# Kernel tuning notes

Hardware: AMD Instinct MI355X
Metric: run time of the kernel (lower is better)

## Reference

```python
import jax, jax.numpy as jnp
import numpy as np

N = 50000   # nodes
E = 800000  # edges
F = 64      # edge_feat_dim == input node dim
H0, H1 = 128, 64  # hidden_dims
OUT = 2
EPS = 1e-5


def _glorot(key, shape):
    limit = float(np.sqrt(6.0 / (shape[0] + shape[1])))
    return jax.random.uniform(key, shape, minval=-limit, maxval=limit, dtype=jnp.float32)


def _layer_norm(h, g, b):
    m = jnp.mean(h, axis=-1, keepdims=True)
    v = jnp.var(h, axis=-1, keepdims=True)
    return (h - m) * jax.lax.rsqrt(v + EPS) * g + b


def setup_inputs() -> dict:
    key = jax.random.key(0)
    ks = jax.random.split(key, 10)
    x = jax.random.normal(ks[0], (N, F), dtype=jnp.float32)
    edge_index = jax.random.randint(ks[1], (2, E), 0, N, dtype=jnp.int64)
    edge_attr = jax.random.normal(ks[2], (E, F), dtype=jnp.float32)
    # conv layer 0: Linear(F + F -> H0); conv layer 1: Linear(H0 + F -> H1)
    W0 = _glorot(ks[3], (F + F, H0)); b0 = jnp.zeros((H0,), jnp.float32)
    W1 = _glorot(ks[4], (H0 + F, H1)); b1 = jnp.zeros((H1,), jnp.float32)
    g0 = jnp.ones((H0,), jnp.float32); be0 = jnp.zeros((H0,), jnp.float32)
    g1 = jnp.ones((H1,), jnp.float32); be1 = jnp.zeros((H1,), jnp.float32)
    # classifier: Linear(2*H1 -> H1) -> ReLU -> Linear(H1 -> OUT)
    Wc0 = _glorot(ks[5], (2 * H1, H1)); bc0 = jnp.zeros((H1,), jnp.float32)
    Wc1 = _glorot(ks[6], (H1, OUT)); bc1 = jnp.zeros((OUT,), jnp.float32)
    return dict(x=x, edge_index=edge_index, edge_attr=edge_attr,
                W0=W0, b0=b0, g0=g0, be0=be0,
                W1=W1, b1=b1, g1=g1, be1=be1,
                Wc0=Wc0, bc0=bc0, Wc1=Wc1, bc1=bc1)


def reference(x, edge_index, edge_attr, W0, b0, g0, be0, W1, b1, g1, be1, Wc0, bc0, Wc1, bc1):
    src, dst = edge_index[0], edge_index[1]
    # scatter-mean of edge_attr per destination node (same for both layers,
    # since edge_attr never changes -> compute once)
    agg_sum = jax.ops.segment_sum(edge_attr, dst, num_segments=N)  # [N, F]
    cnt = jax.ops.segment_sum(jnp.ones((E, 1), x.dtype), dst, num_segments=N)
    agg = agg_sum / jnp.maximum(cnt, 1.0)
    # layer 0: cat -> linear -> relu -> layernorm (dropout is identity at eval)
    h = jax.nn.relu(jnp.concatenate([x, agg], axis=-1) @ W0 + b0)
    h = _layer_norm(h, g0, be0)
    # layer 1
    h = jax.nn.relu(jnp.concatenate([h, agg], axis=-1) @ W1 + b1)
    z = _layer_norm(h, g1, be1)  # [N, H1]
    # edge classifier: gather src/dst embeddings, concat, MLP
    edge_emb = jnp.concatenate([z[src], z[dst]], axis=-1)  # [E, 2*H1]
    hidden = jax.nn.relu(edge_emb @ Wc0 + bc0)
    return hidden @ Wc1 + bc1  # [E, OUT]
```

## Files before the change

kernel.cpp:

```cpp
#include <hip/hip_runtime.h>
#include <hip/hip_bf16.h>

#define N_NODES 50000
#define N_EDGES 800000
#define EPS 1e-5f
#define SCAN_BLOCKS 49

typedef __attribute__((ext_vector_type(8))) short short8;
typedef __attribute__((ext_vector_type(4))) float f32x4;

static __device__ __forceinline__ unsigned short f2bf(float f) {
  union { float f; unsigned u; } v; v.f = f;
  const unsigned r = v.u + 0x7FFF + ((v.u >> 16) & 1);
  return (unsigned short)(r >> 16);
}

__global__ void __launch_bounds__(256) k_prepw(
    const float* __restrict__ W0, const float* __restrict__ W1,
    const float* __restrict__ Wc0,
    unsigned short* __restrict__ W0T, unsigned short* __restrict__ W1T,
    unsigned short* __restrict__ Wc0T) {
  const int idx = blockIdx.x * 256 + threadIdx.x;
  if (idx < 128 * 128) {
    const int n = idx >> 7, k = idx & 127;
    W0T[idx] = f2bf(W0[k * 128 + n]);
  }
  if (idx < 64 * 192) {
    const int n = idx / 192, k = idx - n * 192;
    W1T[idx] = f2bf(W1[k * 64 + n]);
  }
  if (idx < 64 * 128) {
    const int n = idx >> 7, k = idx & 127;
    Wc0T[idx] = f2bf(Wc0[k * 64 + n]);
  }
}

__global__ void __launch_bounds__(256) k_zero(int* __restrict__ cnt) {
  const int base = blockIdx.x * 1024 + threadIdx.x * 4;
  if (base + 3 < N_NODES) {
    *(int4*)(cnt + base) = make_int4(0, 0, 0, 0);
  } else {
    for (int i = 0; i < 4; ++i)
      if (base + i < N_NODES) cnt[base + i] = 0;
  }
}

__global__ void k_count(const int* __restrict__ ei, int* __restrict__ cnt) {
  const int e = blockIdx.x * blockDim.x + threadIdx.x;
  if (e < N_EDGES) atomicAdd(&cnt[ei[N_EDGES + e]], 1);
}

__global__ void __launch_bounds__(256) k_scan_blk(const int* __restrict__ cnt,
                                                  int* __restrict__ starts,
                                                  int* __restrict__ bsum) {
  __shared__ int lds[256];
  const int t = threadIdx.x, b = blockIdx.x;
  const int base = b * 1024 + t * 4;
  int c0 = 0, c1 = 0, c2 = 0, c3 = 0;
  if (base + 3 < N_NODES) {
    const int4 c = *(const int4*)(cnt + base);
    c0 = c.x; c1 = c.y; c2 = c.z; c3 = c.w;
  } else {
    if (base + 0 < N_NODES) c0 = cnt[base + 0];
    if (base + 1 < N_NODES) c1 = cnt[base + 1];
    if (base + 2 < N_NODES) c2 = cnt[base + 2];
    if (base + 3 < N_NODES) c3 = cnt[base + 3];
  }
  const int s = c0 + c1 + c2 + c3;
  lds[t] = s;
  __syncthreads();
  for (int off = 1; off < 256; off <<= 1) {
    const int v = (t >= off) ? lds[t - off] : 0;
    __syncthreads();
    lds[t] += v;
    __syncthreads();
  }
  int run = lds[t] - s;
  if (t == 255) bsum[b] = lds[255];
  const int o0 = run; run += c0;
  const int o1 = run; run += c1;
  const int o2 = run; run += c2;
  const int o3 = run;
  if (base + 3 < N_NODES) {
    *(int4*)(starts + base) = make_int4(o0, o1, o2, o3);
  } else {
    if (base + 0 < N_NODES) starts[base + 0] = o0;
    if (base + 1 < N_NODES) starts[base + 1] = o1;
    if (base + 2 < N_NODES) starts[base + 2] = o2;
    if (base + 3 < N_NODES) starts[base + 3] = o3;
  }
}

__global__ void __launch_bounds__(64) k_scan_top(int* __restrict__ bsum) {
  const int t = threadIdx.x;
  int v = (t < SCAN_BLOCKS) ? bsum[t] : 0;
  const int orig = v;
  for (int off = 1; off < 64; off <<= 1) {
    const int u = __shfl_up(v, off);
    if (t >= off) v += u;
  }
  if (t < SCAN_BLOCKS) bsum[t] = v - orig;
}

__global__ void __launch_bounds__(256) k_scan_add(int* __restrict__ starts,
                                                  int* __restrict__ pos,
                                                  const int* __restrict__ bsum) {
  const int t = threadIdx.x, b = blockIdx.x;
  const int off = bsum[b];
  const int base = b * 1024 + t * 4;
  if (base + 3 < N_NODES) {
    int4 v = *(const int4*)(starts + base);
    v.x += off; v.y += off; v.z += off; v.w += off;
    *(int4*)(starts + base) = v;
    *(int4*)(pos + base) = v;
  } else {
    for (int i = 0; i < 4; ++i)
      if (base + i < N_NODES) {
        const int v = starts[base + i] + off;
        starts[base + i] = v;
        pos[base + i] = v;
      }
  }
  if (b == 0 && t == 0) starts[N_NODES] = N_EDGES;
}

__global__ void k_place(const int* __restrict__ ei, int* __restrict__ pos,
                        int* __restrict__ csr) {
  const int e = blockIdx.x * blockDim.x + threadIdx.x;
  if (e < N_EDGES) {
    const int d = ei[N_EDGES + e];
    const int slot = atomicAdd(&pos[d], 1);
    csr[slot] = e;
  }
}

__global__ void __launch_bounds__(256) k_gather(const float* __restrict__ ea,
                                                const int* __restrict__ csr,
                                                const int* __restrict__ starts,
                                                unsigned short* __restrict__ aggb) {
  const int lane = threadIdx.x & 63;
  const int wv = threadIdx.x >> 6;
  const int wstride = gridDim.x * 4;
  for (int n = blockIdx.x * 4 + wv; n < N_NODES; n += wstride) {
    const int s0 = starts[n], s1 = starts[n + 1];
    float sum = 0.0f;
    int i = s0;
    for (; i + 3 < s1; i += 4) {
      const int e0 = csr[i], e1 = csr[i + 1], e2 = csr[i + 2], e3 = csr[i + 3];
      const float a0 = ea[(size_t)e0 * 64 + lane];
      const float a1 = ea[(size_t)e1 * 64 + lane];
      const float a2 = ea[(size_t)e2 * 64 + lane];
      const float a3 = ea[(size_t)e3 * 64 + lane];
      sum += (a0 + a1) + (a2 + a3);
    }
    for (; i < s1; ++i) sum += ea[(size_t)csr[i] * 64 + lane];
    const int deg = s1 - s0;
    aggb[(size_t)n * 64 + lane] = f2bf(sum / (float)max(deg, 1));
  }
}

__global__ void __launch_bounds__(256) k_nodes(
    const float* __restrict__ x, const unsigned short* __restrict__ aggb,
    const unsigned short* __restrict__ W0T, const float* __restrict__ b0,
    const float* __restrict__ g0, const float* __restrict__ be0,
    const unsigned short* __restrict__ W1T, const float* __restrict__ b1,
    const float* __restrict__ g1, const float* __restrict__ be1,
    unsigned short* __restrict__ zb) {
  __shared__ char A0[64 * 256];
  __shared__ char A1[64 * 384];
  __shared__ float red0[64][4], red1[64][4];

  const int t = threadIdx.x;
  const int lane = t & 63;
  const int w = t >> 6;
  const int m = lane & 15;
  const int g = lane >> 4;
  const int nbase = blockIdx.x * 64;

  {
    const int row = t >> 2, seg = t & 3;
    const int node = nbase + row;
    const int swz = (row & 7) << 4;
    unsigned short h[16];
    if (node < N_NODES) {
      const float4* xr = (const float4*)(x + (size_t)node * 64 + seg * 16);
#pragma unroll
      for (int i = 0; i < 4; ++i) {
        const float4 v = xr[i];
        h[4 * i + 0] = f2bf(v.x); h[4 * i + 1] = f2bf(v.y);
        h[4 * i + 2] = f2bf(v.z); h[4 * i + 3] = f2bf(v.w);
      }
    } else {
#pragma unroll
      for (int i = 0; i < 16; ++i) h[i] = 0;
    }
    uint4 lo, hi;
    unsigned* lp = (unsigned*)&lo;
    unsigned* hp = (unsigned*)&hi;
#pragma unroll
    for (int i = 0; i < 4; ++i) lp[i] = (unsigned)h[2 * i] | ((unsigned)h[2 * i + 1] << 16);
#pragma unroll
    for (int i = 0; i < 4; ++i) hp[i] = (unsigned)h[8 + 2 * i] | ((unsigned)h[8 + 2 * i + 1] << 16);
    *(uint4*)(A0 + row * 256 + ((seg * 32) ^ swz)) = lo;
    *(uint4*)(A0 + row * 256 + ((seg * 32 + 16) ^ swz)) = hi;
    uint4 a0v = make_uint4(0, 0, 0, 0), a1v = make_uint4(0, 0, 0, 0);
    if (node < N_NODES) {
      const uint4* ap = (const uint4*)(aggb + (size_t)node * 64 + seg * 16);
      a0v = ap[0]; a1v = ap[1];
    }
    *(uint4*)(A0 + row * 256 + ((128 + seg * 32) ^ swz)) = a0v;
    *(uint4*)(A0 + row * 256 + ((128 + seg * 32 + 16) ^ swz)) = a1v;
    *(uint4*)(A1 + row * 384 + ((256 + seg * 32) ^ swz)) = a0v;
    *(uint4*)(A1 + row * 384 + ((256 + seg * 32 + 16) ^ swz)) = a1v;
  }

  short8 B0[4][2];
#pragma unroll
  for (int ks = 0; ks < 4; ++ks)
#pragma unroll
    for (int nt = 0; nt < 2; ++nt) {
      const int n = w * 32 + nt * 16 + m;
      B0[ks][nt] = *(const short8*)(W0T + n * 128 + ks * 32 + 8 * g);
    }

  __syncthreads();

  f32x4 acc0[4][2];
#pragma unroll
  for (int mt = 0; mt < 4; ++mt)
#pragma unroll
    for (int nt = 0; nt < 2; ++nt) acc0[mt][nt] = (f32x4){0.f, 0.f, 0.f, 0.f};
#pragma unroll
  for (int ks = 0; ks < 4; ++ks)
#pragma unroll
    for (int mt = 0; mt < 4; ++mt) {
      const int row = 16 * mt + m;
      const short8 a = *(const short8*)(A0 + row * 256 + ((ks * 64 + g * 16) ^ ((row & 7) << 4)));
      acc0[mt][0] = __builtin_amdgcn_mfma_f32_16x16x32_bf16(a, B0[ks][0], acc0[mt][0], 0, 0, 0);
      acc0[mt][1] = __builtin_amdgcn_mfma_f32_16x16x32_bf16(a, B0[ks][1], acc0[mt][1], 0, 0, 0);
    }

  float b0c[2], g0c[2], be0c[2];
#pragma unroll
  for (int nt = 0; nt < 2; ++nt) {
    const int c = w * 32 + nt * 16 + m;
    b0c[nt] = b0[c]; g0c[nt] = g0[c]; be0c[nt] = be0[c];
  }
  float ps1[4][4], ps2[4][4];
#pragma unroll
  for (int mt = 0; mt < 4; ++mt)
#pragma unroll
    for (int q = 0; q < 4; ++q) {
      const float v0 = fmaxf(acc0[mt][0][q] + b0c[0], 0.f);
      const float v1 = fmaxf(acc0[mt][1][q] + b0c[1], 0.f);
      ps1[mt][q] = v0 + v1;
      ps2[mt][q] = v0 * v0 + v1 * v1;
    }
#pragma unroll
  for (int mask = 1; mask <= 8; mask <<= 1)
#pragma unroll
    for (int mt = 0; mt < 4; ++mt)
#pragma unroll
      for (int q = 0; q < 4; ++q) {
        ps1[mt][q] += __shfl_xor(ps1[mt][q], mask);
        ps2[mt][q] += __shfl_xor(ps2[mt][q], mask);
      }
  if (m == 0) {
#pragma unroll
    for (int mt = 0; mt < 4; ++mt)
#pragma unroll
      for (int q = 0; q < 4; ++q) {
        const int row = 16 * mt + 4 * g + q;
        red0[row][w] = ps1[mt][q];
        red1[row][w] = ps2[mt][q];
      }
  }
  __syncthreads();

#pragma unroll
  for (int mt = 0; mt < 4; ++mt)
#pragma unroll
    for (int q = 0; q < 4; ++q) {
      const int row = 16 * mt + 4 * g + q;
      const float4 r0 = *(const float4*)red0[row];
      const float4 r1 = *(const float4*)red1[row];
      const float S1 = (r0.x + r0.y) + (r0.z + r0.w);
      const float S2 = (r1.x + r1.y) + (r1.z + r1.w);
      const float mean = S1 * (1.0f / 128.0f);
      const float var = S2 * (1.0f / 128.0f) - mean * mean;
      const float inv = rsqrtf(var + EPS);
#pragma unroll
      for (int nt = 0; nt < 2; ++nt) {
        const float v = fmaxf(acc0[mt][nt][q] + b0c[nt], 0.f);
        const float o = (v - mean) * inv * g0c[nt] + be0c[nt];
        const int col = w * 32 + nt * 16 + m;
        *(unsigned short*)(A1 + row * 384 + ((2 * col) ^ ((row & 7) << 4))) = f2bf(o);
      }
    }

  short8 B1[6];
  {
    const int n = w * 16 + m;
#pragma unroll
    for (int ks = 0; ks < 6; ++ks)
      B1[ks] = *(const short8*)(W1T + n * 192 + ks * 32 + 8 * g);
  }
  __syncthreads();

  f32x4 acc1[4];
#pragma unroll
  for (int mt = 0; mt < 4; ++mt) acc1[mt] = (f32x4){0.f, 0.f, 0.f, 0.f};
#pragma unroll
  for (int ks = 0; ks < 6; ++ks)
#pragma unroll
    for (int mt = 0; mt < 4; ++mt) {
      const int row = 16 * mt + m;
      const short8 a = *(const short8*)(A1 + row * 384 + ((ks * 64 + g * 16) ^ ((row & 7) << 4)));
      acc1[mt] = __builtin_amdgcn_mfma_f32_16x16x32_bf16(a, B1[ks], acc1[mt], 0, 0, 0);
    }

  const int c1i = w * 16 + m;
  const float b1c = b1[c1i], g1c = g1[c1i], be1c = be1[c1i];
  float qs1[4][4], qs2[4][4];
#pragma unroll
  for (int mt = 0; mt < 4; ++mt)
#pragma unroll
    for (int q = 0; q < 4; ++q) {
      const float v = fmaxf(acc1[mt][q] + b1c, 0.f);
      qs1[mt][q] = v;
      qs2[mt][q] = v * v;
    }
#pragma unroll
  for (int mask = 1; mask <= 8; mask <<= 1)
#pragma unroll
    for (int mt = 0; mt < 4; ++mt)
#pragma unroll
      for (int q = 0; q < 4; ++q) {
        qs1[mt][q] += __shfl_xor(qs1[mt][q], mask);
        qs2[mt][q] += __shfl_xor(qs2[mt][q], mask);
      }
  if (m == 0) {
#pragma unroll
    for (int mt = 0; mt < 4; ++mt)
#pragma unroll
      for (int q = 0; q < 4; ++q) {
        const int row = 16 * mt + 4 * g + q;
        red0[row][w] = qs1[mt][q];
        red1[row][w] = qs2[mt][q];
      }
  }
  __syncthreads();
#pragma unroll
  for (int mt = 0; mt < 4; ++mt)
#pragma unroll
    for (int q = 0; q < 4; ++q) {
      const int row = 16 * mt + 4 * g + q;
      const int node = nbase + row;
      const float4 r0 = *(const float4*)red0[row];
      const float4 r1 = *(const float4*)red1[row];
      const float S1 = (r0.x + r0.y) + (r0.z + r0.w);
      const float S2 = (r1.x + r1.y) + (r1.z + r1.w);
      const float mean = S1 * (1.0f / 64.0f);
      const float var = S2 * (1.0f / 64.0f) - mean * mean;
      const float inv = rsqrtf(var + EPS);
      const float v = fmaxf(acc1[mt][q] + b1c, 0.f);
      const float o = (v - mean) * inv * g1c + be1c;
      if (node < N_NODES) zb[(size_t)node * 64 + c1i] = f2bf(o);
    }
}

__global__ void __launch_bounds__(256) k_cls_mfma(
    const unsigned short* __restrict__ zb, const int* __restrict__ ei,
    const unsigned short* __restrict__ Wc0T, const float* __restrict__ bc0,
    const float* __restrict__ Wc1, const float* __restrict__ bc1,
    float* __restrict__ out) {
  __shared__ unsigned short atile[64 * 128];
  const int t = threadIdx.x;
  const int lane = t & 63;
  const int w = t >> 6;
  const int m = lane & 15;
  const int g = lane >> 4;

  short8 bfrag[4][4];
#pragma unroll
  for (int ks = 0; ks < 4; ++ks)
#pragma unroll
    for (int nt = 0; nt < 4; ++nt)
      bfrag[ks][nt] = *(const short8*)(Wc0T + (nt * 16 + m) * 128 + ks * 32 + 8 * g);
  float wc1v0[4], wc1v1[4], bc0v[4];
#pragma unroll
  for (int nt = 0; nt < 4; ++nt) {
    const int j = nt * 16 + m;
    wc1v0[nt] = Wc1[j * 2 + 0];
    wc1v1[nt] = Wc1[j * 2 + 1];
    bc0v[nt] = bc0[j];
  }
  const float ob0 = bc1[0], ob1 = bc1[1];

  for (int tile = blockIdx.x; tile < N_EDGES / 64; tile += gridDim.x) {
    const int ebase = tile * 64;
#pragma unroll
    for (int ro = 0; ro < 4; ++ro) {
      const int hr = ro * 32 + (t >> 3);
      const int el = hr >> 1, half = hr & 1;
      const int e = ebase + el;
      const int node = half ? ei[N_EDGES + e] : ei[e];
      const uint4 v = *(const uint4*)(zb + (size_t)node * 64 + (t & 7) * 8);
      const int col = (half * 128 + (t & 7) * 16) ^ ((el & 7) << 4);
      *(uint4*)((char*)atile + el * 256 + col) = v;
    }
    __syncthreads();

    f32x4 acc0 = {0.f, 0.f, 0.f, 0.f}, acc1 = acc0, acc2 = acc0, acc3 = acc0;
#pragma unroll
    for (int ks = 0; ks < 4; ++ks) {
      const int row = w * 16 + m;
      const int col = (ks * 64 + g * 16) ^ ((row & 7) << 4);
      const short8 a = *(const short8*)((const char*)atile + row * 256 + col);
      acc0 = __builtin_amdgcn_mfma_f32_16x16x32_bf16(a, bfrag[ks][0], acc0, 0, 0, 0);
      acc1 = __builtin_amdgcn_mfma_f32_16x16x32_bf16(a, bfrag[ks][1], acc1, 0, 0, 0);
      acc2 = __builtin_amdgcn_mfma_f32_16x16x32_bf16(a, bfrag[ks][2], acc2, 0, 0, 0);
      acc3 = __builtin_amdgcn_mfma_f32_16x16x32_bf16(a, bfrag[ks][3], acc3, 0, 0, 0);
    }
    float p0[4], p1[4];
#pragma unroll
    for (int r = 0; r < 4; ++r) {
      const float h0v = fmaxf(acc0[r] + bc0v[0], 0.f);
      const float h1v = fmaxf(acc1[r] + bc0v[1], 0.f);
      const float h2v = fmaxf(acc2[r] + bc0v[2], 0.f);
      const float h3v = fmaxf(acc3[r] + bc0v[3], 0.f);
      p0[r] = h0v * wc1v0[0] + h1v * wc1v0[1] + h2v * wc1v0[2] + h3v * wc1v0[3];
      p1[r] = h0v * wc1v1[0] + h1v * wc1v1[1] + h2v * wc1v1[2] + h3v * wc1v1[3];
    }
#pragma unroll
    for (int mask = 1; mask <= 8; mask <<= 1)
#pragma unroll
      for (int r = 0; r < 4; ++r) {
        p0[r] += __shfl_xor(p0[r], mask);
        p1[r] += __shfl_xor(p1[r], mask);
      }
    const int eout = ebase + w * 16 + g * 4;
#pragma unroll
    for (int r = 0; r < 4; ++r) {
      if (m == 2 * r) out[(size_t)(eout + r) * 2 + 0] = p0[r] + ob0;
      if (m == 2 * r + 1) out[(size_t)(eout + r) * 2 + 1] = p1[r] + ob1;
    }
    __syncthreads();
  }
}

extern "C" void kernel_launch(void* const* d_in, const int* in_sizes, int n_in,
                              void* d_out, int out_size, void* d_ws, size_t ws_size,
                              hipStream_t stream) {
  const float* x   = (const float*)d_in[0];
  const int*   ei  = (const int*)d_in[1];
  const float* ea  = (const float*)d_in[2];
  const float* W0  = (const float*)d_in[3];
  const float* b0  = (const float*)d_in[4];
  const float* g0  = (const float*)d_in[5];
  const float* be0 = (const float*)d_in[6];
  const float* W1  = (const float*)d_in[7];
  const float* b1  = (const float*)d_in[8];
  const float* g1  = (const float*)d_in[9];
  const float* be1 = (const float*)d_in[10];
  const float* Wc0 = (const float*)d_in[11];
  const float* bc0 = (const float*)d_in[12];
  const float* Wc1 = (const float*)d_in[13];
  const float* bc1 = (const float*)d_in[14];
  float* out = (float*)d_out;

  char* base = (char*)d_ws;
  unsigned short* zb   = (unsigned short*)base;
  unsigned short* aggb = zb + (size_t)N_NODES * 64;
  unsigned short* W0T  = aggb + (size_t)N_NODES * 64;
  unsigned short* W1T  = W0T + 128 * 128;
  unsigned short* Wc0T = W1T + 64 * 192;
  int* cnt    = (int*)(Wc0T + 64 * 128);
  int* starts = cnt + N_NODES;
  int* pos    = starts + N_NODES + 4;
  int* bsum   = pos + N_NODES;
  int* csr    = bsum + 64;

  k_prepw<<<64, 256, 0, stream>>>(W0, W1, Wc0, W0T, W1T, Wc0T);
  k_zero<<<SCAN_BLOCKS, 256, 0, stream>>>(cnt);
  k_count<<<(N_EDGES + 255) / 256, 256, 0, stream>>>(ei, cnt);
  k_scan_blk<<<SCAN_BLOCKS, 256, 0, stream>>>(cnt, starts, bsum);
  k_scan_top<<<1, 64, 0, stream>>>(bsum);
  k_scan_add<<<SCAN_BLOCKS, 256, 0, stream>>>(starts, pos, bsum);
  k_place<<<(N_EDGES + 255) / 256, 256, 0, stream>>>(ei, pos, csr);
  k_gather<<<12500, 256, 0, stream>>>(ea, csr, starts, aggb);
  k_nodes<<<(N_NODES + 63) / 64, 256, 0, stream>>>(x, aggb, W0T, b0, g0, be0,
                                                   W1T, b1, g1, be1, zb);
  k_cls_mfma<<<2048, 256, 0, stream>>>(zb, ei, Wc0T, bc0, Wc1, bc1, out);
}
```

Before: 226.8 us.

## Fold zero and top-scan kernels into neighbors; load classifier A fragments directly from global

Zeroing of the count array moves into the weight-prep kernel, and the block-sum scan moves into the scan-add kernel, where each block reduces the preceding block sums with a wave shuffle. This removes two kernel launches. The edge classifier no longer stages gathered embeddings through shared memory: each wave handles 16 edges and loads MFMA A fragments straight from global memory, which removes the LDS round trip and the block barriers. In exchange, global gathers are less coalesced, with each lane reading 16-byte pieces of node rows.

```diff
diff --git a/kernel.cpp b/kernel.cpp
--- a/kernel.cpp
+++ b/kernel.cpp
@@ -19,7 +19,7 @@
     const float* __restrict__ W0, const float* __restrict__ W1,
     const float* __restrict__ Wc0,
     unsigned short* __restrict__ W0T, unsigned short* __restrict__ W1T,
-    unsigned short* __restrict__ Wc0T) {
+    unsigned short* __restrict__ Wc0T, int* __restrict__ cnt) {
   const int idx = blockIdx.x * 256 + threadIdx.x;
   if (idx < 128 * 128) {
     const int n = idx >> 7, k = idx & 127;
@@ -33,16 +33,7 @@
     const int n = idx >> 7, k = idx & 127;
     Wc0T[idx] = f2bf(Wc0[k * 64 + n]);
   }
-}
-
-__global__ void __launch_bounds__(256) k_zero(int* __restrict__ cnt) {
-  const int base = blockIdx.x * 1024 + threadIdx.x * 4;
-  if (base + 3 < N_NODES) {
-    *(int4*)(cnt + base) = make_int4(0, 0, 0, 0);
-  } else {
-    for (int i = 0; i < 4; ++i)
-      if (base + i < N_NODES) cnt[base + i] = 0;
-  }
+  for (int i = idx; i < N_NODES; i += 64 * 256) cnt[i] = 0;
 }
 
 __global__ void k_count(const int* __restrict__ ei, int* __restrict__ cnt) {
@@ -91,22 +82,18 @@
   }
 }
 
-__global__ void __launch_bounds__(64) k_scan_top(int* __restrict__ bsum) {
-  const int t = threadIdx.x;
-  int v = (t < SCAN_BLOCKS) ? bsum[t] : 0;
-  const int orig = v;
-  for (int off = 1; off < 64; off <<= 1) {
-    const int u = __shfl_up(v, off);
-    if (t >= off) v += u;
-  }
-  if (t < SCAN_BLOCKS) bsum[t] = v - orig;
-}
-
 __global__ void __launch_bounds__(256) k_scan_add(int* __restrict__ starts,
                                                   int* __restrict__ pos,
                                                   const int* __restrict__ bsum) {
+  __shared__ int s_off;
   const int t = threadIdx.x, b = blockIdx.x;
-  const int off = bsum[b];
+  if (t < 64) {
+    int v = (t < b) ? bsum[t] : 0;
+    for (int o = 32; o; o >>= 1) v += __shfl_xor(v, o);
+    if (t == 0) s_off = v;
+  }
+  __syncthreads();
+  const int off = s_off;
   const int base = b * 1024 + t * 4;
   if (base + 3 < N_NODES) {
     int4 v = *(const int4*)(starts + base);
@@ -374,7 +361,6 @@
     const unsigned short* __restrict__ Wc0T, const float* __restrict__ bc0,
     const float* __restrict__ Wc1, const float* __restrict__ bc1,
     float* __restrict__ out) {
-  __shared__ unsigned short atile[64 * 128];
   const int t = threadIdx.x;
   const int lane = t & 63;
   const int w = t >> 6;
@@ -397,31 +383,34 @@
   }
   const float ob0 = bc1[0], ob1 = bc1[1];
 
-  for (int tile = blockIdx.x; tile < N_EDGES / 64; tile += gridDim.x) {
-    const int ebase = tile * 64;
-#pragma unroll
-    for (int ro = 0; ro < 4; ++ro) {
-      const int hr = ro * 32 + (t >> 3);
-      const int el = hr >> 1, half = hr & 1;
-      const int e = ebase + el;
-      const int node = half ? ei[N_EDGES + e] : ei[e];
-      const uint4 v = *(const uint4*)(zb + (size_t)node * 64 + (t & 7) * 8);
-      const int col = (half * 128 + (t & 7) * 16) ^ ((el & 7) << 4);
-      *(uint4*)((char*)atile + el * 256 + col) = v;
-    }
-    __syncthreads();
+  const int gstride = gridDim.x * 4;
+  for (int grp = blockIdx.x * 4 + w; grp < N_EDGES / 16; grp += gstride) {
+    const int ebase = grp * 16;
+    const int e = ebase + m;
+    const int s = ei[e], d = ei[N_EDGES + e];
+    const short8 a0 = *(const short8*)(zb + (size_t)s * 64 + 8 * g);
+    const short8 a1 = *(const short8*)(zb + (size_t)s * 64 + 32 + 8 * g);
+    const short8 a2 = *(const short8*)(zb + (size_t)d * 64 + 8 * g);
+    const short8 a3 = *(const short8*)(zb + (size_t)d * 64 + 32 + 8 * g);
 
     f32x4 acc0 = {0.f, 0.f, 0.f, 0.f}, acc1 = acc0, acc2 = acc0, acc3 = acc0;
-#pragma unroll
-    for (int ks = 0; ks < 4; ++ks) {
-      const int row = w * 16 + m;
-      const int col = (ks * 64 + g * 16) ^ ((row & 7) << 4);
-      const short8 a = *(const short8*)((const char*)atile + row * 256 + col);
-      acc0 = __builtin_amdgcn_mfma_f32_16x16x32_bf16(a, bfrag[ks][0], acc0, 0, 0, 0);
-      acc1 = __builtin_amdgcn_mfma_f32_16x16x32_bf16(a, bfrag[ks][1], acc1, 0, 0, 0);
-      acc2 = __builtin_amdgcn_mfma_f32_16x16x32_bf16(a, bfrag[ks][2], acc2, 0, 0, 0);
-      acc3 = __builtin_amdgcn_mfma_f32_16x16x32_bf16(a, bfrag[ks][3], acc3, 0, 0, 0);
-    }
+    acc0 = __builtin_amdgcn_mfma_f32_16x16x32_bf16(a0, bfrag[0][0], acc0, 0, 0, 0);
+    acc1 = __builtin_amdgcn_mfma_f32_16x16x32_bf16(a0, bfrag[0][1], acc1, 0, 0, 0);
+    acc2 = __builtin_amdgcn_mfma_f32_16x16x32_bf16(a0, bfrag[0][2], acc2, 0, 0, 0);
+    acc3 = __builtin_amdgcn_mfma_f32_16x16x32_bf16(a0, bfrag[0][3], acc3, 0, 0, 0);
+    acc0 = __builtin_amdgcn_mfma_f32_16x16x32_bf16(a1, bfrag[1][0], acc0, 0, 0, 0);
+    acc1 = __builtin_amdgcn_mfma_f32_16x16x32_bf16(a1, bfrag[1][1], acc1, 0, 0, 0);
+    acc2 = __builtin_amdgcn_mfma_f32_16x16x32_bf16(a1, bfrag[1][2], acc2, 0, 0, 0);
+    acc3 = __builtin_amdgcn_mfma_f32_16x16x32_bf16(a1, bfrag[1][3], acc3, 0, 0, 0);
+    acc0 = __builtin_amdgcn_mfma_f32_16x16x32_bf16(a2, bfrag[2][0], acc0, 0, 0, 0);
+    acc1 = __builtin_amdgcn_mfma_f32_16x16x32_bf16(a2, bfrag[2][1], acc1, 0, 0, 0);
+    acc2 = __builtin_amdgcn_mfma_f32_16x16x32_bf16(a2, bfrag[2][2], acc2, 0, 0, 0);
+    acc3 = __builtin_amdgcn_mfma_f32_16x16x32_bf16(a2, bfrag[2][3], acc3, 0, 0, 0);
+    acc0 = __builtin_amdgcn_mfma_f32_16x16x32_bf16(a3, bfrag[3][0], acc0, 0, 0, 0);
+    acc1 = __builtin_amdgcn_mfma_f32_16x16x32_bf16(a3, bfrag[3][1], acc1, 0, 0, 0);
+    acc2 = __builtin_amdgcn_mfma_f32_16x16x32_bf16(a3, bfrag[3][2], acc2, 0, 0, 0);
+    acc3 = __builtin_amdgcn_mfma_f32_16x16x32_bf16(a3, bfrag[3][3], acc3, 0, 0, 0);
+
     float p0[4], p1[4];
 #pragma unroll
     for (int r = 0; r < 4; ++r) {
@@ -439,13 +428,12 @@
         p0[r] += __shfl_xor(p0[r], mask);
         p1[r] += __shfl_xor(p1[r], mask);
       }
-    const int eout = ebase + w * 16 + g * 4;
+    const int eout = ebase + g * 4;
 #pragma unroll
     for (int r = 0; r < 4; ++r) {
       if (m == 2 * r) out[(size_t)(eout + r) * 2 + 0] = p0[r] + ob0;
       if (m == 2 * r + 1) out[(size_t)(eout + r) * 2 + 1] = p1[r] + ob1;
     }
-    __syncthreads();
   }
 }
 
@@ -481,11 +469,9 @@
   int* bsum   = pos + N_NODES;
   int* csr    = bsum + 64;
 
-  k_prepw<<<64, 256, 0, stream>>>(W0, W1, Wc0, W0T, W1T, Wc0T);
-  k_zero<<<SCAN_BLOCKS, 256, 0, stream>>>(cnt);
+  k_prepw<<<64, 256, 0, stream>>>(W0, W1, Wc0, W0T, W1T, Wc0T, cnt);
   k_count<<<(N_EDGES + 255) / 256, 256, 0, stream>>>(ei, cnt);
   k_scan_blk<<<SCAN_BLOCKS, 256, 0, stream>>>(cnt, starts, bsum);
-  k_scan_top<<<1, 64, 0, stream>>>(bsum);
   k_scan_add<<<SCAN_BLOCKS, 256, 0, stream>>>(starts, pos, bsum);
   k_place<<<(N_EDGES + 255) / 256, 256, 0, stream>>>(ei, pos, csr);
   k_gather<<<12500, 256, 0, stream>>>(ea, csr, starts, aggb);
```

Measured after the change: 213.8 us. 5.7% less time.
